# Optimization experiments

Measured on AMD Instinct MI355X. Metric: run time of the kernel, lower is better.

## Reference

```python
import jax, jax.numpy as jnp
import numpy as np
import math

NUM_POSE_FEAT = 64  # -> pos emb dim 128
N_NBR = 16
TEMP = 10000.0


def pos2posemb2d(pos, num_pos_feats=NUM_POSE_FEAT):
    # PETR-style 2D sine embedding; pos: (..., 2) in [0,1)
    scale = 2.0 * math.pi
    pos = pos * scale
    dim_t = jnp.arange(num_pos_feats, dtype=pos.dtype)
    dim_t = TEMP ** (2.0 * jnp.floor(dim_t / 2.0) / num_pos_feats)
    pos_x = pos[..., 0:1] / dim_t  # (..., P)
    pos_y = pos[..., 1:2] / dim_t

    def interleave(p):
        return jnp.stack([jnp.sin(p[..., 0::2]), jnp.cos(p[..., 1::2])], axis=-1).reshape(p.shape[:-1] + (-1,))

    return jnp.concatenate([interleave(pos_y), interleave(pos_x)], axis=-1)  # (..., 2P)


def mlp(x, W1, b1, W2, b2):
    return jax.nn.relu(x @ W1 + b1) @ W2 + b2


def setup_inputs() -> dict:
    key = jax.random.key(0)
    ks = jax.random.split(key, 12)
    B, S, L, D, P2 = 4, 4096, 8192, 256, 2 * NUM_POSE_FEAT
    s1 = 1.0 / np.sqrt(P2)
    s2 = 1.0 / np.sqrt(D)
    return {
        "memory": jax.random.normal(ks[0], (B, L, D), jnp.float32),
        "mem_coor": jax.random.uniform(ks[1], (B, L, 2), dtype=jnp.float32),
        "q_coor": jax.random.uniform(ks[2], (B, S, 2), dtype=jnp.float32),
        "Wq1": jax.random.normal(ks[3], (P2, D), jnp.float32) * s1,
        "bq1": jnp.zeros((D,), jnp.float32),
        "Wq2": jax.random.normal(ks[4], (D, D), jnp.float32) * s2,
        "bq2": jnp.zeros((D,), jnp.float32),
        "Wk1": jax.random.normal(ks[5], (P2, D), jnp.float32) * s1,
        "bk1": jnp.zeros((D,), jnp.float32),
        "Wk2": jax.random.normal(ks[6], (D, D), jnp.float32) * s2,
        "bk2": jnp.zeros((D,), jnp.float32),
        "B": 4,
    }


def reference(memory, mem_coor, q_coor, Wq1, bq1, Wq2, bq2, Wk1, bk1, Wk2, bk2, B):
    # memory: (B, L, D); mem_coor: (B, L, 2); q_coor: (B, S, 2)
    Bn, L, D = memory.shape
    query = mlp(pos2posemb2d(q_coor), Wq1, bq1, Wq2, bq2)      # (B, S, D) query = query_pos
    mem_pos = mlp(pos2posemb2d(mem_coor), Wk1, bk1, Wk2, bk2)  # (B, L, D)
    kv_pe = mem_pos + memory                                   # (B, L, D)

    # squared pairwise distances via matmul expansion (monotonic in true distance,
    # only the top-k ORDER is consumed downstream)
    q2 = jnp.sum(q_coor * q_coor, axis=-1)                     # (B, S)
    m2 = jnp.sum(mem_coor * mem_coor, axis=-1)                 # (B, L)
    d2 = q2[:, :, None] + m2[:, None, :] - 2.0 * jnp.einsum("bsc,blc->bsl", q_coor, mem_coor)
    _, idx = jax.lax.top_k(-d2, N_NBR)                         # (B, S, k) nearest-neighbor indices

    bidx = jnp.arange(Bn)[:, None, None]
    kv_m = kv_pe[bidx, idx]                                    # (B, S, k, D) gathered pos-embedded memory
    prod = query[:, :, None, :] * kv_m / jnp.sqrt(jnp.asarray(D, query.dtype))
    attn = jax.nn.softmax(prod, axis=-1)                       # softmax over feature dim D
    out = attn * memory[bidx, idx]                             # (B, S, k, D)
    return out
```

## Files before the change

kernel.cpp:

```cpp
#include <hip/hip_runtime.h>
#include <math.h>

#define NB 4
#define NS 4096
#define NL 8192
#define ND 256
#define NP2 128
#define NK 16

#define GCELLS 32
#define GH 0.03125f
#define CAP 256
#define EPSM 2e-5f

__device__ __forceinline__ float sum_sq_np(float x, float y) {
#pragma clang fp contract(off)
  return x * x + y * y;
}

__device__ __forceinline__ float dist2_fast(float q2, float m2, float qx, float qy,
                                            float mx, float my) {
#pragma clang fp contract(off)
  float dot = __builtin_fmaf(qy, my, qx * mx);
  float s = q2 + m2;
  return __builtin_fmaf(-2.0f, dot, s);
}

__device__ __forceinline__ unsigned f32ord(float f) {
  unsigned u = __float_as_uint(f);
  return u ^ ((unsigned)((int)u >> 31) | 0x80000000u);
}

template <int NR>
__device__ __forceinline__ unsigned extract16(const unsigned long long* candrow,
                                              int cnt, int lane,
                                              int* __restrict__ outp) {
  unsigned long long myc[NR];
#pragma unroll
  for (int j = 0; j < NR; ++j) {
    int p = lane + j * 64;
    myc[j] = (p < cnt) ? candrow[p] : ~0ull;
  }
  unsigned tau_ord = 0xffffffffu;
#pragma unroll 1
  for (int r = 0; r < NK; ++r) {
    unsigned long long m = myc[0];
#pragma unroll
    for (int j = 1; j < NR; ++j) m = myc[j] < m ? myc[j] : m;
#pragma unroll
    for (int o = 1; o < 64; o <<= 1) {
      unsigned long long other = __shfl_xor(m, o, 64);
      if (other < m) m = other;
    }
    if (lane == 0) outp[r] = (int)(unsigned)(m & 0xffffffffull);
    if (r == NK - 1) tau_ord = (unsigned)(m >> 32);
#pragma unroll
    for (int j = 0; j < NR; ++j)
      if (myc[j] == m) myc[j] = ~0ull;
  }
  return tau_ord;
}

#define RPAD 20
#define NSBLK (NB * NS / 16)

struct __align__(16) MlpSmem {
  union {
    float pe[NP2][RPAD];
    float h[ND][RPAD];
  };
};

__device__ __forceinline__ void fma4row(float4& a, float p, const float4& w) {
  a.x = fmaf(p, w.x, a.x);
  a.y = fmaf(p, w.y, a.y);
  a.z = fmaf(p, w.z, a.z);
  a.w = fmaf(p, w.w, a.w);
}

__device__ __forceinline__ void consume4v(const float (*L)[RPAD], int k0,
                                          const float4* w, float4* acc) {
#pragma unroll
  for (int u = 0; u < 4; ++u) {
    int k = k0 + u;
    float4 p0 = *(const float4*)&L[k][0];
    float4 p1 = *(const float4*)&L[k][4];
    float4 p2 = *(const float4*)&L[k][8];
    float4 p3 = *(const float4*)&L[k][12];
    float4 wu = w[u];
    fma4row(acc[0],  p0.x, wu); fma4row(acc[1],  p0.y, wu);
    fma4row(acc[2],  p0.z, wu); fma4row(acc[3],  p0.w, wu);
    fma4row(acc[4],  p1.x, wu); fma4row(acc[5],  p1.y, wu);
    fma4row(acc[6],  p1.z, wu); fma4row(acc[7],  p1.w, wu);
    fma4row(acc[8],  p2.x, wu); fma4row(acc[9],  p2.y, wu);
    fma4row(acc[10], p2.z, wu); fma4row(acc[11], p2.w, wu);
    fma4row(acc[12], p3.x, wu); fma4row(acc[13], p3.y, wu);
    fma4row(acc[14], p3.z, wu); fma4row(acc[15], p3.w, wu);
  }
}

__global__ __launch_bounds__(64) void mlp_fused_kernel(
    const float* __restrict__ q_coor, const float* __restrict__ mem_coor,
    const float* __restrict__ memory,
    const float* __restrict__ Wq1, const float* __restrict__ bq1,
    const float* __restrict__ Wq2, const float* __restrict__ bq2,
    const float* __restrict__ Wk1, const float* __restrict__ bk1,
    const float* __restrict__ Wk2, const float* __restrict__ bk2,
    float* __restrict__ query, float* __restrict__ kv_pe) {
  __shared__ MlpSmem sm;
  const int tid = threadIdx.x;
  const int bid = blockIdx.x;
  const bool isS = bid < NSBLK;
  const float* coor = isS ? q_coor : mem_coor;
  const float* W1 = isS ? Wq1 : Wk1;
  const float* b1 = isS ? bq1 : bk1;
  const float* W2 = isS ? Wq2 : Wk2;
  const float* b2 = isS ? bq2 : bk2;
  const float* addmem = isS ? (const float*)nullptr : memory;
  float* out = isS ? query : kv_pe;
  const int row0 = (isS ? bid : bid - NSBLK) * 16;
  const int c0 = tid * 4;

#pragma unroll
  for (int it = 0; it < 16; ++it) {
    int e = tid + it * 64;
    int r = e >> 6;
    int rem = e & 63;
    int part = rem >> 5;
    int j = rem & 31;
    float c = coor[(size_t)(row0 + r) * 2 + (part ^ 1)];
    float inv_t = exp2f((float)j * -0.4152410118609718f);
    float arg = c * 6.2831853071795864f * inv_t;
    float sv, cv;
    sincosf(arg, &sv, &cv);
    int k0 = part * 64 + 2 * j;
    sm.pe[k0][r] = sv;
    sm.pe[k0 + 1][r] = cv;
  }
  __syncthreads();

  float4 acc[16];
  float4 wA[4], wB[4];
  {
    float4 bb = *(const float4*)&b1[c0];
#pragma unroll
    for (int r = 0; r < 16; ++r) acc[r] = bb;
  }
#pragma unroll
  for (int u = 0; u < 4; ++u)
    wA[u] = *(const float4*)&W1[(size_t)u * ND + c0];
#pragma unroll 1
  for (int k0 = 0; k0 < NP2; k0 += 8) {
#pragma unroll
    for (int u = 0; u < 4; ++u)
      wB[u] = *(const float4*)&W1[(size_t)(k0 + 4 + u) * ND + c0];
    consume4v(sm.pe, k0, wA, acc);
    if (k0 + 8 < NP2) {
#pragma unroll
      for (int u = 0; u < 4; ++u)
        wA[u] = *(const float4*)&W1[(size_t)(k0 + 8 + u) * ND + c0];
    }
    consume4v(sm.pe, k0 + 4, wB, acc);
  }
  __syncthreads();
#pragma unroll
  for (int r = 0; r < 16; ++r) {
    sm.h[c0 + 0][r] = fmaxf(acc[r].x, 0.0f);
    sm.h[c0 + 1][r] = fmaxf(acc[r].y, 0.0f);
    sm.h[c0 + 2][r] = fmaxf(acc[r].z, 0.0f);
    sm.h[c0 + 3][r] = fmaxf(acc[r].w, 0.0f);
  }
  __syncthreads();

  {
    float4 bb = *(const float4*)&b2[c0];
#pragma unroll
    for (int r = 0; r < 16; ++r) acc[r] = bb;
  }
#pragma unroll
  for (int u = 0; u < 4; ++u)
    wA[u] = *(const float4*)&W2[(size_t)u * ND + c0];
#pragma unroll 1
  for (int k0 = 0; k0 < ND; k0 += 8) {
#pragma unroll
    for (int u = 0; u < 4; ++u)
      wB[u] = *(const float4*)&W2[(size_t)(k0 + 4 + u) * ND + c0];
    consume4v(sm.h, k0, wA, acc);
    if (k0 + 8 < ND) {
#pragma unroll
      for (int u = 0; u < 4; ++u)
        wA[u] = *(const float4*)&W2[(size_t)(k0 + 8 + u) * ND + c0];
    }
    consume4v(sm.h, k0 + 4, wB, acc);
  }
#pragma unroll
  for (int r = 0; r < 16; ++r) {
    size_t g = (size_t)(row0 + r);
    float4 v = acc[r];
    if (addmem) {
      float4 mm = *(const float4*)&addmem[g * ND + c0];
      v.x += mm.x; v.y += mm.y; v.z += mm.z; v.w += mm.w;
    }
    *(float4*)&out[g * ND + c0] = v;
  }
}

__global__ __launch_bounds__(1024) void build_kernel(
    const float* __restrict__ mem_coor, const float* __restrict__ q_coor,
    float4* __restrict__ sorted, int* __restrict__ starts,
    int* __restrict__ qord) {
  __shared__ int hist[GCELLS * GCELLS];
  __shared__ int cur[GCELLS * GCELLS];
  const int bid = blockIdx.x;
  const bool isMem = bid < NB;
  const int b = isMem ? bid : bid - NB;
  const int n = isMem ? NL : NS;
  const float2* cc = (const float2*)(isMem ? mem_coor : q_coor) + (size_t)b * n;
  const int tid = threadIdx.x;

  hist[tid] = 0;
  __syncthreads();
  for (int it = 0; it < n / 1024; ++it) {
    float2 c = cc[it * 1024 + tid];
    int cx = (int)(c.x * 32.0f); cx = cx > 31 ? 31 : cx;
    int cy = (int)(c.y * 32.0f); cy = cy > 31 ? 31 : cy;
    atomicAdd(&hist[cy * GCELLS + cx], 1);
  }
  __syncthreads();
  const int own = hist[tid];
  for (int o = 1; o < 1024; o <<= 1) {
    int v = (tid >= o) ? hist[tid - o] : 0;
    __syncthreads();
    hist[tid] += v;
    __syncthreads();
  }
  const int excl = hist[tid] - own;
  if (isMem) {
    starts[b * (GCELLS * GCELLS + 1) + tid] = excl;
    if (tid == 0) starts[b * (GCELLS * GCELLS + 1) + GCELLS * GCELLS] = NL;
  }
  cur[tid] = excl;
  __syncthreads();
  for (int it = 0; it < n / 1024; ++it) {
    int i = it * 1024 + tid;
    float2 c = cc[i];
    int cx = (int)(c.x * 32.0f); cx = cx > 31 ? 31 : cx;
    int cy = (int)(c.y * 32.0f); cy = cy > 31 ? 31 : cy;
    int pos = atomicAdd(&cur[cy * GCELLS + cx], 1);
    if (isMem) {
      sorted[(size_t)b * NL + pos] =
          make_float4(c.x, c.y, sum_sq_np(c.x, c.y), __int_as_float(i));
    } else {
      qord[b * NS + pos] = i;
    }
  }
}

__global__ __launch_bounds__(256) void topk_kernel(
    const float* __restrict__ q_coor, const float4* __restrict__ sorted,
    const int* __restrict__ starts, int* __restrict__ idx_out) {
  __shared__ unsigned long long cand[4][CAP];
  __shared__ int fcnt[4];

  const int tid = threadIdx.x;
  const int wv = tid >> 6;
  const int lane = tid & 63;
  const int qi = blockIdx.x * 4 + wv;
  const int b = qi >> 12;

  const float qx = q_coor[(size_t)qi * 2 + 0];
  const float qy = q_coor[(size_t)qi * 2 + 1];
  const float q2 = sum_sq_np(qx, qy);
  const float4* sp = sorted + (size_t)b * NL;
  const int* st = starts + b * (GCELLS * GCELLS + 1);
  int* outp = idx_out + (size_t)qi * NK;

  int ci = (int)(qx * 32.0f); ci = ci > 31 ? 31 : ci;
  int cj = (int)(qy * 32.0f); cj = cj > 31 ? 31 : cj;

  int x0 = ci - 1 < 0 ? 0 : ci - 1, x1 = ci + 1 > 31 ? 31 : ci + 1;
  int y0 = cj - 1 < 0 ? 0 : cj - 1, y1 = cj + 1 > 31 ? 31 : cj + 1;
  int cnt = 0;
  bool ovf = false;

  auto span = [&](int y, int xa, int xb) {
    int s0 = st[y * GCELLS + xa];
    int e0 = st[y * GCELLS + xb + 1];
    int len = e0 - s0;
    if (cnt + len > CAP) { ovf = true; return; }
    for (int i = lane; i < len; i += 64) {
      float4 rx = sp[s0 + i];
      float d2 = dist2_fast(q2, rx.z, qx, qy, rx.x, rx.y);
      cand[wv][cnt + i] = ((unsigned long long)f32ord(d2) << 32) |
                          (unsigned)__float_as_int(rx.w);
    }
    cnt += len;
  };

  for (int y = y0; y <= y1 && !ovf; ++y) span(y, x0, x1);

  int R = 1;
  while (!ovf) {
    unsigned tau_ord;
    if (cnt <= 128) tau_ord = extract16<2>(cand[wv], cnt, lane, outp);
    else            tau_ord = extract16<4>(cand[wv], cnt, lane, outp);
    float dxl = x0 > 0  ? qx - (float)x0 * GH        : 1e30f;
    float dxr = x1 < 31 ? (float)(x1 + 1) * GH - qx  : 1e30f;
    float dyl = y0 > 0  ? qy - (float)y0 * GH        : 1e30f;
    float dyr = y1 < 31 ? (float)(y1 + 1) * GH - qy  : 1e30f;
    float dmin = fminf(fminf(dxl, dxr), fminf(dyl, dyr));
    float bound = dmin * dmin - EPSM;
    if (cnt >= NK && tau_ord < f32ord(bound)) return;
    if (x0 == 0 && x1 == 31 && y0 == 0 && y1 == 31) return;
    ++R;
    int nx0 = ci - R < 0 ? 0 : ci - R, nx1 = ci + R > 31 ? 31 : ci + R;
    int ny0 = cj - R < 0 ? 0 : cj - R, ny1 = cj + R > 31 ? 31 : cj + R;
    if (ny0 < y0) span(ny0, nx0, nx1);
    if (ny1 > y1 && !ovf) span(ny1, nx0, nx1);
    for (int y = y0; y <= y1 && !ovf; ++y) {
      if (nx0 < x0) span(y, nx0, x0 - 1);
      if (nx1 > x1 && !ovf) span(y, x1 + 1, nx1);
    }
    x0 = nx0; x1 = nx1; y0 = ny0; y1 = ny1;
  }

  float lmin = __builtin_inff();
#pragma unroll 8
  for (int it = 0; it < NL / 64; ++it) {
    float4 rx = sp[it * 64 + lane];
    float d2 = dist2_fast(q2, rx.z, qx, qy, rx.x, rx.y);
    lmin = fminf(lmin, d2);
  }
  float tau;
  {
    float curm = lmin;
    for (int r = 0; r < NK; ++r) {
      float m = curm;
#pragma unroll
      for (int o = 1; o < 64; o <<= 1) m = fminf(m, __shfl_xor(m, o, 64));
      tau = m;
      if (curm == m) curm = __builtin_inff();
    }
  }
  if (lane == 0) fcnt[wv] = 0;
#pragma unroll 4
  for (int it = 0; it < NL / 64; ++it) {
    float4 rx = sp[it * 64 + lane];
    float d2 = dist2_fast(q2, rx.z, qx, qy, rx.x, rx.y);
    bool hit = (d2 <= tau);
    unsigned long long mask = __ballot(hit);
    if (mask) {
      int base = fcnt[wv];
      if (hit) {
        int pos = base + (int)__popcll(mask & ((1ull << lane) - 1ull));
        if (pos < CAP) {
          cand[wv][pos] = ((unsigned long long)f32ord(d2) << 32) |
                          (unsigned)__float_as_int(rx.w);
        }
      }
      if (lane == 0) fcnt[wv] = base + (int)__popcll(mask);
    }
  }
  int N = fcnt[wv];
  if (N > CAP) N = CAP;
  extract16<4>(cand[wv], N, lane, outp);
}

__global__ __launch_bounds__(256) void attn_kernel(
    const float* __restrict__ query, const float* __restrict__ kv_pe,
    const float* __restrict__ memory, const int* __restrict__ idx,
    const int* __restrict__ qord, float* __restrict__ out) {
  const int tid = threadIdx.x;
  const int wv = tid >> 6;
  const int lane = tid & 63;
  const int bid = ((blockIdx.x & 7) * (NB * NS / 4 / 8)) + (blockIdx.x >> 3);
  const int qpos = bid * 4 + wv;
  const int b = qpos >> 12;
  const int qi = b * NS + qord[qpos];

  float4 q4 = *(const float4*)(query + (size_t)qi * ND + lane * 4);
  int lv = 0;
  if (lane < NK) lv = idx[(size_t)qi * NK + lane];

#pragma unroll 4
  for (int k = 0; k < NK; ++k) {
    int l = __shfl(lv, k, 64);
    size_t base = ((size_t)b * NL + l) * ND + (size_t)lane * 4;
    float4 kv = *(const float4*)(kv_pe + base);
    float4 mm = *(const float4*)(memory + base);
    float p0 = q4.x * kv.x * 0.0625f;
    float p1 = q4.y * kv.y * 0.0625f;
    float p2 = q4.z * kv.z * 0.0625f;
    float p3 = q4.w * kv.w * 0.0625f;
    float mx = fmaxf(fmaxf(p0, p1), fmaxf(p2, p3));
#pragma unroll
    for (int o = 1; o < 64; o <<= 1) mx = fmaxf(mx, __shfl_xor(mx, o, 64));
    float e0 = expf(p0 - mx);
    float e1 = expf(p1 - mx);
    float e2 = expf(p2 - mx);
    float e3 = expf(p3 - mx);
    float s = (e0 + e1) + (e2 + e3);
#pragma unroll
    for (int o = 1; o < 64; o <<= 1) s += __shfl_xor(s, o, 64);
    float inv = 1.0f / s;
    float4 o4;
    o4.x = e0 * inv * mm.x;
    o4.y = e1 * inv * mm.y;
    o4.z = e2 * inv * mm.z;
    o4.w = e3 * inv * mm.w;
    *(float4*)(out + ((size_t)qi * NK + k) * ND + (size_t)lane * 4) = o4;
  }
}

extern "C" void kernel_launch(void* const* d_in, const int* in_sizes, int n_in,
                              void* d_out, int out_size, void* d_ws, size_t ws_size,
                              hipStream_t stream) {
  (void)in_sizes; (void)n_in; (void)out_size; (void)ws_size;
  const float* memory   = (const float*)d_in[0];
  const float* mem_coor = (const float*)d_in[1];
  const float* q_coor   = (const float*)d_in[2];
  const float* Wq1 = (const float*)d_in[3];
  const float* bq1 = (const float*)d_in[4];
  const float* Wq2 = (const float*)d_in[5];
  const float* bq2 = (const float*)d_in[6];
  const float* Wk1 = (const float*)d_in[7];
  const float* bk1 = (const float*)d_in[8];
  const float* Wk2 = (const float*)d_in[9];
  const float* bk2 = (const float*)d_in[10];

  float* query = (float*)d_ws;
  float* kv_pe = query + (size_t)NB * NS * ND;
  int*   nidx  = (int*)(kv_pe + (size_t)NB * NL * ND);
  int*   qord  = nidx + (size_t)NB * NS * NK;
  float* outp  = (float*)d_out;

  float4* sorted  = (float4*)d_out;
  int*    gstarts = (int*)((char*)d_out + (size_t)NB * NL * 16);

  hipLaunchKernelGGL(build_kernel, dim3(2 * NB), dim3(1024), 0, stream,
                     mem_coor, q_coor, sorted, gstarts, qord);
  hipLaunchKernelGGL(mlp_fused_kernel, dim3(NSBLK + NB * NL / 16), dim3(64),
                     0, stream, q_coor, mem_coor, memory,
                     Wq1, bq1, Wq2, bq2, Wk1, bk1, Wk2, bk2, query, kv_pe);
  hipLaunchKernelGGL(topk_kernel, dim3(NB * NS / 4), dim3(256), 0, stream,
                     q_coor, sorted, gstarts, nidx);
  hipLaunchKernelGGL(attn_kernel, dim3(NB * NS / 4), dim3(256), 0, stream,
                     query, kv_pe, memory, nidx, qord, outp);
}
```

Before: 521.6 us.

## Fuse neighbor top-k search into attention kernel via shared-memory indices

Merges the grid-based top-k kernel with the attention kernel so that each wave's selected neighbor indices stay in shared memory instead of going through global memory. Queries are now processed in the spatially sorted order, which may improve cache reuse of the sorted memory coordinates. The sorted and grid buffers move from the output buffer into workspace, since the fused kernel writes the output while still reading them. This removes one kernel launch and the index round-trip, at the cost of a heavier kernel with more registers and less overlap between search and attention phases.

```diff
diff --git a/kernel.cpp b/kernel.cpp
--- a/kernel.cpp
+++ b/kernel.cpp
@@ -34,7 +34,7 @@
 template <int NR>
 __device__ __forceinline__ unsigned extract16(const unsigned long long* candrow,
                                               int cnt, int lane,
-                                              int* __restrict__ outp) {
+                                              int* __restrict__ idxsel) {
   unsigned long long myc[NR];
 #pragma unroll
   for (int j = 0; j < NR; ++j) {
@@ -52,7 +52,7 @@
       unsigned long long other = __shfl_xor(m, o, 64);
       if (other < m) m = other;
     }
-    if (lane == 0) outp[r] = (int)(unsigned)(m & 0xffffffffull);
+    if (lane == 0) idxsel[r] = (int)(unsigned)(m & 0xffffffffull);
     if (r == NK - 1) tau_ord = (unsigned)(m >> 32);
 #pragma unroll
     for (int j = 0; j < NR; ++j)
@@ -256,24 +256,29 @@
   }
 }
 
-__global__ __launch_bounds__(256) void topk_kernel(
+__global__ __launch_bounds__(256) void topk_attn_kernel(
     const float* __restrict__ q_coor, const float4* __restrict__ sorted,
-    const int* __restrict__ starts, int* __restrict__ idx_out) {
+    const int* __restrict__ starts, const int* __restrict__ qord,
+    const float* __restrict__ query, const float* __restrict__ kv_pe,
+    const float* __restrict__ memory, float* __restrict__ out) {
   __shared__ unsigned long long cand[4][CAP];
   __shared__ int fcnt[4];
+  __shared__ int idxsel[4][NK];
 
   const int tid = threadIdx.x;
   const int wv = tid >> 6;
   const int lane = tid & 63;
-  const int qi = blockIdx.x * 4 + wv;
-  const int b = qi >> 12;
+  const int bid = ((blockIdx.x & 7) * (NB * NS / 4 / 8)) + (blockIdx.x >> 3);
+  const int qpos = bid * 4 + wv;
+  const int b = qpos >> 12;
+  const int qi = b * NS + qord[qpos];
 
   const float qx = q_coor[(size_t)qi * 2 + 0];
   const float qy = q_coor[(size_t)qi * 2 + 1];
   const float q2 = sum_sq_np(qx, qy);
   const float4* sp = sorted + (size_t)b * NL;
   const int* st = starts + b * (GCELLS * GCELLS + 1);
-  int* outp = idx_out + (size_t)qi * NK;
+  int* isel = idxsel[wv];
 
   int ci = (int)(qx * 32.0f); ci = ci > 31 ? 31 : ci;
   int cj = (int)(qy * 32.0f); cj = cj > 31 ? 31 : cj;
@@ -299,19 +304,20 @@
 
   for (int y = y0; y <= y1 && !ovf; ++y) span(y, x0, x1);
 
+  bool done = false;
   int R = 1;
-  while (!ovf) {
+  while (!ovf && !done) {
     unsigned tau_ord;
-    if (cnt <= 128) tau_ord = extract16<2>(cand[wv], cnt, lane, outp);
-    else            tau_ord = extract16<4>(cand[wv], cnt, lane, outp);
+    if (cnt <= 128) tau_ord = extract16<2>(cand[wv], cnt, lane, isel);
+    else            tau_ord = extract16<4>(cand[wv], cnt, lane, isel);
     float dxl = x0 > 0  ? qx - (float)x0 * GH        : 1e30f;
     float dxr = x1 < 31 ? (float)(x1 + 1) * GH - qx  : 1e30f;
     float dyl = y0 > 0  ? qy - (float)y0 * GH        : 1e30f;
     float dyr = y1 < 31 ? (float)(y1 + 1) * GH - qy  : 1e30f;
     float dmin = fminf(fminf(dxl, dxr), fminf(dyl, dyr));
     float bound = dmin * dmin - EPSM;
-    if (cnt >= NK && tau_ord < f32ord(bound)) return;
-    if (x0 == 0 && x1 == 31 && y0 == 0 && y1 == 31) return;
+    if (cnt >= NK && tau_ord < f32ord(bound)) { done = true; break; }
+    if (x0 == 0 && x1 == 31 && y0 == 0 && y1 == 31) { done = true; break; }
     ++R;
     int nx0 = ci - R < 0 ? 0 : ci - R, nx1 = ci + R > 31 ? 31 : ci + R;
     int ny0 = cj - R < 0 ? 0 : cj - R, ny1 = cj + R > 31 ? 31 : cj + R;
@@ -324,67 +330,54 @@
     x0 = nx0; x1 = nx1; y0 = ny0; y1 = ny1;
   }
 
-  float lmin = __builtin_inff();
+  if (!done) {
+    float lmin = __builtin_inff();
 #pragma unroll 8
-  for (int it = 0; it < NL / 64; ++it) {
-    float4 rx = sp[it * 64 + lane];
-    float d2 = dist2_fast(q2, rx.z, qx, qy, rx.x, rx.y);
-    lmin = fminf(lmin, d2);
-  }
-  float tau;
-  {
-    float curm = lmin;
-    for (int r = 0; r < NK; ++r) {
-      float m = curm;
-#pragma unroll
-      for (int o = 1; o < 64; o <<= 1) m = fminf(m, __shfl_xor(m, o, 64));
-      tau = m;
-      if (curm == m) curm = __builtin_inff();
-    }
-  }
-  if (lane == 0) fcnt[wv] = 0;
+    for (int it = 0; it < NL / 64; ++it) {
+      float4 rx = sp[it * 64 + lane];
+      float d2 = dist2_fast(q2, rx.z, qx, qy, rx.x, rx.y);
+      lmin = fminf(lmin, d2);
+    }
+    float tau;
+    {
+      float curm = lmin;
+      for (int r = 0; r < NK; ++r) {
+        float m = curm;
+#pragma unroll
+        for (int o = 1; o < 64; o <<= 1) m = fminf(m, __shfl_xor(m, o, 64));
+        tau = m;
+        if (curm == m) curm = __builtin_inff();
+      }
+    }
+    if (lane == 0) fcnt[wv] = 0;
 #pragma unroll 4
-  for (int it = 0; it < NL / 64; ++it) {
-    float4 rx = sp[it * 64 + lane];
-    float d2 = dist2_fast(q2, rx.z, qx, qy, rx.x, rx.y);
-    bool hit = (d2 <= tau);
-    unsigned long long mask = __ballot(hit);
-    if (mask) {
-      int base = fcnt[wv];
-      if (hit) {
-        int pos = base + (int)__popcll(mask & ((1ull << lane) - 1ull));
-        if (pos < CAP) {
-          cand[wv][pos] = ((unsigned long long)f32ord(d2) << 32) |
-                          (unsigned)__float_as_int(rx.w);
+    for (int it = 0; it < NL / 64; ++it) {
+      float4 rx = sp[it * 64 + lane];
+      float d2 = dist2_fast(q2, rx.z, qx, qy, rx.x, rx.y);
+      bool hit = (d2 <= tau);
+      unsigned long long mask = __ballot(hit);
+      if (mask) {
+        int base = fcnt[wv];
+        if (hit) {
+          int pos = base + (int)__popcll(mask & ((1ull << lane) - 1ull));
+          if (pos < CAP) {
+            cand[wv][pos] = ((unsigned long long)f32ord(d2) << 32) |
+                            (unsigned)__float_as_int(rx.w);
+          }
         }
+        if (lane == 0) fcnt[wv] = base + (int)__popcll(mask);
       }
-      if (lane == 0) fcnt[wv] = base + (int)__popcll(mask);
-    }
-  }
-  int N = fcnt[wv];
-  if (N > CAP) N = CAP;
-  extract16<4>(cand[wv], N, lane, outp);
-}
-
-__global__ __launch_bounds__(256) void attn_kernel(
-    const float* __restrict__ query, const float* __restrict__ kv_pe,
-    const float* __restrict__ memory, const int* __restrict__ idx,
-    const int* __restrict__ qord, float* __restrict__ out) {
-  const int tid = threadIdx.x;
-  const int wv = tid >> 6;
-  const int lane = tid & 63;
-  const int bid = ((blockIdx.x & 7) * (NB * NS / 4 / 8)) + (blockIdx.x >> 3);
-  const int qpos = bid * 4 + wv;
-  const int b = qpos >> 12;
-  const int qi = b * NS + qord[qpos];
+    }
+    int N = fcnt[wv];
+    if (N > CAP) N = CAP;
+    extract16<4>(cand[wv], N, lane, isel);
+  }
 
   float4 q4 = *(const float4*)(query + (size_t)qi * ND + lane * 4);
-  int lv = 0;
-  if (lane < NK) lv = idx[(size_t)qi * NK + lane];
 
 #pragma unroll 4
   for (int k = 0; k < NK; ++k) {
-    int l = __shfl(lv, k, 64);
+    int l = isel[k];
     size_t base = ((size_t)b * NL + l) * ND + (size_t)lane * 4;
     float4 kv = *(const float4*)(kv_pe + base);
     float4 mm = *(const float4*)(memory + base);
@@ -430,20 +423,18 @@
 
   float* query = (float*)d_ws;
   float* kv_pe = query + (size_t)NB * NS * ND;
-  int*   nidx  = (int*)(kv_pe + (size_t)NB * NL * ND);
-  int*   qord  = nidx + (size_t)NB * NS * NK;
+  int*   qord  = (int*)(kv_pe + (size_t)NB * NL * ND);
   float* outp  = (float*)d_out;
 
-  float4* sorted  = (float4*)d_out;
-  int*    gstarts = (int*)((char*)d_out + (size_t)NB * NL * 16);
+  float4* sorted  = (float4*)(qord + NB * NS);
+  int*    gstarts = (int*)(sorted + (size_t)NB * NL);
 
   hipLaunchKernelGGL(build_kernel, dim3(2 * NB), dim3(1024), 0, stream,
                      mem_coor, q_coor, sorted, gstarts, qord);
   hipLaunchKernelGGL(mlp_fused_kernel, dim3(NSBLK + NB * NL / 16), dim3(64),
                      0, stream, q_coor, mem_coor, memory,
                      Wq1, bq1, Wq2, bq2, Wk1, bk1, Wk2, bk2, query, kv_pe);
-  hipLaunchKernelGGL(topk_kernel, dim3(NB * NS / 4), dim3(256), 0, stream,
-                     q_coor, sorted, gstarts, nidx);
-  hipLaunchKernelGGL(attn_kernel, dim3(NB * NS / 4), dim3(256), 0, stream,
-                     query, kv_pe, memory, nidx, qord, outp);
-}
+  hipLaunchKernelGGL(topk_attn_kernel, dim3(NB * NS / 4), dim3(256), 0,
+                     stream, q_coor, sorted, gstarts, qord,
+                     query, kv_pe, memory, outp);
+}
```

Measured after the change: 500.4 us. -4.1%, faster.
